# Optimization experiments

Measured on AMD Instinct MI355X. Metric: run time of the kernel, lower is better.

The kernel has to match this reference:

```python
import jax, jax.numpy as jnp
import numpy as np

B, S, H = 8, 4096, 1024
N_IDX = 65536
N_SEG = 8192


def setup_inputs() -> dict:
    key = jax.random.key(0)
    k1, k2, k3, k4, k5 = jax.random.split(key, 5)
    transformer_hidden = jax.random.normal(k1, (B, S, H), dtype=jnp.float32)
    indices = jax.random.randint(k2, (N_IDX,), 0, B * S, dtype=jnp.int32)
    segment_ids = jnp.sort(jax.random.randint(k3, (N_IDX,), 0, N_SEG, dtype=jnp.int32))
    W_dense = jax.random.normal(k4, (H, H), dtype=jnp.float32) * (1.0 / np.sqrt(H))
    b_dense = jnp.zeros((H,), dtype=jnp.float32)
    W_proj = jax.random.normal(k5, (1, H), dtype=jnp.float32) * (1.0 / np.sqrt(H))
    b_proj = jnp.zeros((1,), dtype=jnp.float32)
    return {
        "transformer_hidden": transformer_hidden,
        "indices": indices,
        "segment_ids": segment_ids,
        "W_dense": W_dense,
        "b_dense": b_dense,
        "W_proj": W_proj,
        "b_proj": b_proj,
    }


def reference(transformer_hidden, indices, segment_ids, W_dense, b_dense, W_proj, b_proj):
    # Flatten tokens: [B*S, H]
    hid = transformer_hidden.reshape(-1, transformer_hidden.shape[-1])
    # Ragged gather of grouped token indices, then per-group mean (segment mean)
    gathered = hid[indices]  # [n_idx, H]
    sums = jax.ops.segment_sum(gathered, segment_ids, num_segments=N_SEG)  # [G, H]
    counts = jax.ops.segment_sum(
        jnp.ones((indices.shape[0],), dtype=hid.dtype), segment_ids, num_segments=N_SEG
    )
    h = sums / jnp.maximum(counts, 1.0)[:, None]  # [G, H] group means
    # dense -> gelu (torch exact erf gelu) -> lin_proj -> flatten
    z = jax.nn.gelu(h @ W_dense.T + b_dense, approximate=False)
    predictions = z @ W_proj.T + b_proj  # [G, 1]
    return predictions.reshape(-1)
```

## Files before the change

kernel.cpp:

```cpp
#include <hip/hip_runtime.h>
#include <stdint.h>

#define BH   (8 * 4096)
#define HDIM 1024
#define NIDX 65536
#define NSEG 8192
#define KD   1024
#define ND   1024

typedef __bf16 bf16x8 __attribute__((ext_vector_type(8)));
typedef float  f32x4  __attribute__((ext_vector_type(4)));

__device__ __forceinline__ unsigned short f2bf(float f) {
  unsigned int u = __float_as_uint(f);
  u += 0x7fffu + ((u >> 16) & 1u);
  return (unsigned short)(u >> 16);
}

__device__ __forceinline__ void async16(const void* g, void* l) {
  __builtin_amdgcn_global_load_lds(
      (const __attribute__((address_space(1))) void*)g,
      (__attribute__((address_space(3))) void*)l,
      16, 0, 0);
}

__global__ void convw_kernel(const float* __restrict__ W, unsigned short* __restrict__ Wb) {
  int i = (blockIdx.x * 256 + threadIdx.x) * 4;
  float4 v = *(const float4*)(W + i);
  ushort4 o;
  o.x = f2bf(v.x); o.y = f2bf(v.y); o.z = f2bf(v.z); o.w = f2bf(v.w);
  *(ushort4*)(Wb + i) = o;
}

__global__ void segmean_kernel(const float* __restrict__ hid,
                               const int* __restrict__ indices,
                               const int* __restrict__ seg,
                               unsigned short* __restrict__ hb,
                               float* __restrict__ out,
                               const float* __restrict__ b_proj) {
  const int g = blockIdx.x;
  const int t = threadIdx.x;

  int lo = 0, hi = NIDX;
  while (lo < hi) { int mid = (lo + hi) >> 1; if (seg[mid] < g) lo = mid + 1; else hi = mid; }
  const int start = lo;
  hi = NIDX;
  while (lo < hi) { int mid = (lo + hi) >> 1; if (seg[mid] <= g) lo = mid + 1; else hi = mid; }
  const int end = lo;

  float4 acc = make_float4(0.f, 0.f, 0.f, 0.f);
  for (int i = start; i < end; ++i) {
    int r = indices[i];
    float4 v = *(const float4*)(hid + (size_t)r * HDIM + t * 4);
    acc.x += v.x; acc.y += v.y; acc.z += v.z; acc.w += v.w;
  }
  const float inv = 1.0f / fmaxf((float)(end - start), 1.0f);
  ushort4 o;
  o.x = f2bf(acc.x * inv); o.y = f2bf(acc.y * inv);
  o.z = f2bf(acc.z * inv); o.w = f2bf(acc.w * inv);
  *(ushort4*)(hb + (size_t)g * HDIM + t * 4) = o;

  if (t == 0) out[g] = b_proj[0];
}

__global__ void gemm_gelu_proj_kernel(const unsigned short* __restrict__ A,
                                      const unsigned short* __restrict__ Bw,
                                      const float* __restrict__ b_dense,
                                      const float* __restrict__ w_proj,
                                      float* __restrict__ out) {
  __shared__ alignas(16) unsigned short As[128 * 32];
  __shared__ alignas(16) unsigned short Bs[128 * 32];

  const int tid  = threadIdx.x;
  const int lane = tid & 63;
  const int wave = tid >> 6;
  const int wm   = wave >> 1;
  const int wn   = wave & 1;
  const int m0   = blockIdx.x * 128;
  const int n0   = blockIdx.y * 128;
  const int lr   = lane & 15;
  const int quad = lane >> 4;

  f32x4 acc[4][4];
#pragma unroll
  for (int mi = 0; mi < 4; ++mi)
#pragma unroll
    for (int ni = 0; ni < 4; ++ni) {
      acc[mi][ni][0] = 0.f; acc[mi][ni][1] = 0.f;
      acc[mi][ni][2] = 0.f; acc[mi][ni][3] = 0.f;
    }

  for (int kt = 0; kt < KD / 32; ++kt) {
    const int k0 = kt * 32;
#pragma unroll
    for (int j = 0; j < 2; ++j) {
      int c   = j * 256 + wave * 64 + lane;
      int row = c >> 2, kc = c & 3;
      const unsigned short* ga = A  + (size_t)(m0 + row) * KD + k0 + kc * 8;
      const unsigned short* gb = Bw + (size_t)(n0 + row) * KD + k0 + kc * 8;
      char* lbase_a = (char*)As + (j * 256 + wave * 64) * 16;
      char* lbase_b = (char*)Bs + (j * 256 + wave * 64) * 16;
      async16(ga, lbase_a);
      async16(gb, lbase_b);
    }
    __syncthreads();

    bf16x8 af[4], bf_[4];
#pragma unroll
    for (int i = 0; i < 4; ++i) {
      af[i]  = *(const bf16x8*)(As + (wm * 64 + i * 16 + lr) * 32 + quad * 8);
      bf_[i] = *(const bf16x8*)(Bs + (wn * 64 + i * 16 + lr) * 32 + quad * 8);
    }
#pragma unroll
    for (int mi = 0; mi < 4; ++mi)
#pragma unroll
      for (int ni = 0; ni < 4; ++ni)
        acc[mi][ni] = __builtin_amdgcn_mfma_f32_16x16x32_bf16(af[mi], bf_[ni], acc[mi][ni], 0, 0, 0);
    __syncthreads();
  }

#pragma unroll
  for (int mi = 0; mi < 4; ++mi) {
    float rp[4] = {0.f, 0.f, 0.f, 0.f};
#pragma unroll
    for (int ni = 0; ni < 4; ++ni) {
      int col  = n0 + wn * 64 + ni * 16 + lr;
      float bd = b_dense[col];
      float wp = w_proj[col];
#pragma unroll
      for (int r = 0; r < 4; ++r) {
        float v  = acc[mi][ni][r] + bd;
        float gl = 0.5f * v * (1.0f + erff(v * 0.70710678118654752f));
        rp[r] += gl * wp;
      }
    }
#pragma unroll
    for (int r = 0; r < 4; ++r) {
      float c = rp[r];
      c += __shfl_xor(c, 1);
      c += __shfl_xor(c, 2);
      c += __shfl_xor(c, 4);
      c += __shfl_xor(c, 8);
      if (lr == 0)
        atomicAdd(out + (m0 + wm * 64 + mi * 16 + quad * 4 + r), c);
    }
  }
}

extern "C" void kernel_launch(void* const* d_in, const int* in_sizes, int n_in,
                              void* d_out, int out_size, void* d_ws, size_t ws_size,
                              hipStream_t stream) {
  const float* hid     = (const float*)d_in[0];
  const int*   indices = (const int*)d_in[1];
  const int*   seg     = (const int*)d_in[2];
  const float* W_dense = (const float*)d_in[3];
  const float* b_dense = (const float*)d_in[4];
  const float* W_proj  = (const float*)d_in[5];
  const float* b_proj  = (const float*)d_in[6];
  float* out = (float*)d_out;

  unsigned short* hb = (unsigned short*)d_ws;
  unsigned short* Wb = (unsigned short*)((char*)d_ws + (size_t)NSEG * KD * sizeof(unsigned short));

  convw_kernel<<<dim3((ND * KD) / 1024), 256, 0, stream>>>(W_dense, Wb);
  segmean_kernel<<<dim3(NSEG), 256, 0, stream>>>(hid, indices, seg, hb, out, b_proj);
  gemm_gelu_proj_kernel<<<dim3(NSEG / 128, ND / 128), 256, 0, stream>>>(hb, Wb, b_dense, W_proj, out);
}
```

Baseline: 252.9 us.

## Precompute segment bounds, shrink GEMM N tile, and swizzle LDS layout

Adds a bounds kernel that writes each segment's start offset once, so each segmean block reads two values instead of running two binary searches over the segment array. The GEMM tile narrows from 128x128 to 128x64, which doubles the grid to 1024 blocks for better CU occupancy and halves accumulator registers. An XOR swizzle on the 16-byte chunks in LDS is meant to reduce bank conflicts on fragment reads. The cost is one extra kernel launch, re-reading A twice as often, and more atomics into the output.

```diff
diff --git a/kernel.cpp b/kernel.cpp
--- a/kernel.cpp
+++ b/kernel.cpp
@@ -32,21 +32,24 @@
   *(ushort4*)(Wb + i) = o;
 }
 
+__global__ void bounds_kernel(const int* __restrict__ seg, int* __restrict__ starts) {
+  int i = blockIdx.x * 256 + threadIdx.x;
+  if (i > NIDX) return;
+  int prev = (i == 0) ? -1 : seg[i - 1];
+  int cur  = (i == NIDX) ? NSEG : seg[i];
+  for (int g = prev + 1; g <= cur; ++g) starts[g] = i;
+}
+
 __global__ void segmean_kernel(const float* __restrict__ hid,
                                const int* __restrict__ indices,
-                               const int* __restrict__ seg,
+                               const int* __restrict__ starts,
                                unsigned short* __restrict__ hb,
                                float* __restrict__ out,
                                const float* __restrict__ b_proj) {
   const int g = blockIdx.x;
   const int t = threadIdx.x;
-
-  int lo = 0, hi = NIDX;
-  while (lo < hi) { int mid = (lo + hi) >> 1; if (seg[mid] < g) lo = mid + 1; else hi = mid; }
-  const int start = lo;
-  hi = NIDX;
-  while (lo < hi) { int mid = (lo + hi) >> 1; if (seg[mid] <= g) lo = mid + 1; else hi = mid; }
-  const int end = lo;
+  const int start = starts[g];
+  const int end   = starts[g + 1];
 
   float4 acc = make_float4(0.f, 0.f, 0.f, 0.f);
   for (int i = start; i < end; ++i) {
@@ -63,13 +66,14 @@
   if (t == 0) out[g] = b_proj[0];
 }
 
-__global__ void gemm_gelu_proj_kernel(const unsigned short* __restrict__ A,
-                                      const unsigned short* __restrict__ Bw,
-                                      const float* __restrict__ b_dense,
-                                      const float* __restrict__ w_proj,
-                                      float* __restrict__ out) {
+__global__ void __launch_bounds__(256)
+gemm_gelu_proj_kernel(const unsigned short* __restrict__ A,
+                      const unsigned short* __restrict__ Bw,
+                      const float* __restrict__ b_dense,
+                      const float* __restrict__ w_proj,
+                      float* __restrict__ out) {
   __shared__ alignas(16) unsigned short As[128 * 32];
-  __shared__ alignas(16) unsigned short Bs[128 * 32];
+  __shared__ alignas(16) unsigned short Bs[64 * 32];
 
   const int tid  = threadIdx.x;
   const int lane = tid & 63;
@@ -77,15 +81,15 @@
   const int wm   = wave >> 1;
   const int wn   = wave & 1;
   const int m0   = blockIdx.x * 128;
-  const int n0   = blockIdx.y * 128;
+  const int n0   = blockIdx.y * 64;
   const int lr   = lane & 15;
   const int quad = lane >> 4;
 
-  f32x4 acc[4][4];
+  f32x4 acc[4][2];
 #pragma unroll
   for (int mi = 0; mi < 4; ++mi)
 #pragma unroll
-    for (int ni = 0; ni < 4; ++ni) {
+    for (int ni = 0; ni < 2; ++ni) {
       acc[mi][ni][0] = 0.f; acc[mi][ni][1] = 0.f;
       acc[mi][ni][2] = 0.f; acc[mi][ni][3] = 0.f;
     }
@@ -95,26 +99,37 @@
 #pragma unroll
     for (int j = 0; j < 2; ++j) {
       int c   = j * 256 + wave * 64 + lane;
-      int row = c >> 2, kc = c & 3;
-      const unsigned short* ga = A  + (size_t)(m0 + row) * KD + k0 + kc * 8;
-      const unsigned short* gb = Bw + (size_t)(n0 + row) * KD + k0 + kc * 8;
-      char* lbase_a = (char*)As + (j * 256 + wave * 64) * 16;
-      char* lbase_b = (char*)Bs + (j * 256 + wave * 64) * 16;
-      async16(ga, lbase_a);
-      async16(gb, lbase_b);
+      int row = c >> 2, sl = c & 3;
+      int kcg = sl ^ ((row >> 1) & 3);
+      async16(A + (size_t)(m0 + row) * KD + k0 + kcg * 8,
+              (char*)As + (j * 256 + wave * 64) * 16);
+    }
+    {
+      int c   = wave * 64 + lane;
+      int row = c >> 2, sl = c & 3;
+      int kcg = sl ^ ((row >> 1) & 3);
+      async16(Bw + (size_t)(n0 + row) * KD + k0 + kcg * 8,
+              (char*)Bs + (wave * 64) * 16);
     }
     __syncthreads();
 
-    bf16x8 af[4], bf_[4];
+    bf16x8 af[4], bf_[2];
 #pragma unroll
     for (int i = 0; i < 4; ++i) {
-      af[i]  = *(const bf16x8*)(As + (wm * 64 + i * 16 + lr) * 32 + quad * 8);
-      bf_[i] = *(const bf16x8*)(Bs + (wn * 64 + i * 16 + lr) * 32 + quad * 8);
+      int ra  = wm * 64 + i * 16 + lr;
+      int sla = quad ^ ((ra >> 1) & 3);
+      af[i] = *(const bf16x8*)(As + ra * 32 + sla * 8);
+    }
+#pragma unroll
+    for (int i = 0; i < 2; ++i) {
+      int rb  = wn * 32 + i * 16 + lr;
+      int slb = quad ^ ((rb >> 1) & 3);
+      bf_[i] = *(const bf16x8*)(Bs + rb * 32 + slb * 8);
     }
 #pragma unroll
     for (int mi = 0; mi < 4; ++mi)
 #pragma unroll
-      for (int ni = 0; ni < 4; ++ni)
+      for (int ni = 0; ni < 2; ++ni)
         acc[mi][ni] = __builtin_amdgcn_mfma_f32_16x16x32_bf16(af[mi], bf_[ni], acc[mi][ni], 0, 0, 0);
     __syncthreads();
   }
@@ -123,8 +138,8 @@
   for (int mi = 0; mi < 4; ++mi) {
     float rp[4] = {0.f, 0.f, 0.f, 0.f};
 #pragma unroll
-    for (int ni = 0; ni < 4; ++ni) {
-      int col  = n0 + wn * 64 + ni * 16 + lr;
+    for (int ni = 0; ni < 2; ++ni) {
+      int col  = n0 + wn * 32 + ni * 16 + lr;
       float bd = b_dense[col];
       float wp = w_proj[col];
 #pragma unroll
@@ -159,10 +174,12 @@
   const float* b_proj  = (const float*)d_in[6];
   float* out = (float*)d_out;
 
-  unsigned short* hb = (unsigned short*)d_ws;
-  unsigned short* Wb = (unsigned short*)((char*)d_ws + (size_t)NSEG * KD * sizeof(unsigned short));
+  unsigned short* hb     = (unsigned short*)d_ws;
+  unsigned short* Wb     = (unsigned short*)((char*)d_ws + (size_t)NSEG * KD * 2);
+  int*            starts = (int*)((char*)d_ws + (size_t)NSEG * KD * 2 + (size_t)ND * KD * 2);
 
   convw_kernel<<<dim3((ND * KD) / 1024), 256, 0, stream>>>(W_dense, Wb);
-  segmean_kernel<<<dim3(NSEG), 256, 0, stream>>>(hid, indices, seg, hb, out, b_proj);
-  gemm_gelu_proj_kernel<<<dim3(NSEG / 128, ND / 128), 256, 0, stream>>>(hb, Wb, b_dense, W_proj, out);
+  bounds_kernel<<<dim3((NIDX + 256) / 256), 256, 0, stream>>>(seg, starts);
+  segmean_kernel<<<dim3(NSEG), 256, 0, stream>>>(hid, indices, starts, hb, out, b_proj);
+  gemm_gelu_proj_kernel<<<dim3(NSEG / 128, ND / 64), 256, 0, stream>>>(hb, Wb, b_dense, W_proj, out);
 }
```

Measured after the change: 243.6 us. -3.7%, faster.
